# Kernel optimization log

Measured on AMD Instinct MI355X. Metric: run time of the kernel, lower is better.

The kernel has to match this reference:

```python
import jax, jax.numpy as jnp
import numpy as np

K = 16          # num clusters
DZ = 64         # dim_zt == dim_zi (required by decoder matmul)
DT = 1024       # treatment feature dim (dim_t)
NT = 2048       # number of treatments == dim_x (columns of input_ins)
NI = 4096       # number of instances
MU_P_WT = 5.0
COS_EPS = 1e-6


def setup_inputs() -> dict:
    key = jax.random.key(0)
    ks = jax.random.split(key, 12)
    s = 0.02
    return {
        "input_ins": jax.random.uniform(ks[0], (NI, NT), dtype=jnp.float32),
        "input_treat": jax.random.normal(ks[1], (NT, DT), dtype=jnp.float32),
        # nn.Linear params (torch layout: W [out, in], y = x @ W.T + b)
        "W_mu_zt": jax.random.normal(ks[2], (DZ, DT)) * s,
        "b_mu_zt": jnp.zeros((DZ,), jnp.float32),
        "W_lv_zt": jax.random.normal(ks[3], (DZ, DT)) * s,
        "b_lv_zt": jnp.zeros((DZ,), jnp.float32),
        "W_arec": jax.random.normal(ks[4], (DT, DZ)) * s,
        "b_arec": jnp.zeros((DT,), jnp.float32),
        "W_mu_zi": jax.random.normal(ks[5], (DZ, NT)) * s,
        "b_mu_zi": jnp.zeros((DZ,), jnp.float32),
        "W_lv_zi": jax.random.normal(ks[6], (DZ, NT)) * s,
        "b_lv_zi": jnp.zeros((DZ,), jnp.float32),
        "mu_p_zt": jax.random.normal(ks[7], (K, DZ), dtype=jnp.float32),
        "logvar_p_zt": jnp.ones((K, DZ), jnp.float32),
        "W_y1": jax.random.normal(ks[8], (K * DZ, DZ)) * s,
        "b_y1": jnp.zeros((K * DZ,), jnp.float32),
        "W_y2": jax.random.normal(ks[9], (1, K * DZ)) * s,
        "b_y2": jnp.zeros((1,), jnp.float32),
    }


def reference(input_ins, input_treat, W_mu_zt, b_mu_zt, W_lv_zt, b_lv_zt,
              W_arec, b_arec, W_mu_zi, b_mu_zi, W_lv_zi, b_lv_zi,
              mu_p_zt, logvar_p_zt, W_y1, b_y1, W_y2, b_y2):
    # encode_t (eval mode: zt_sample = mu_zt)
    mu_zt = input_treat @ W_mu_zt.T + b_mu_zt           # [NT, DZ]
    logvar_zt = input_treat @ W_lv_zt.T + b_lv_zt       # [NT, DZ]
    zt = mu_zt

    # compute_qc (cosine similarity vs scaled cluster centers, *10)
    centers = MU_P_WT * mu_p_zt                          # [K, DZ]
    num = zt @ centers.T                                 # [NT, K]
    denom = jnp.maximum(
        jnp.linalg.norm(zt, axis=1, keepdims=True) * jnp.linalg.norm(centers, axis=1)[None, :],
        COS_EPS)
    qc_raw = 10.0 * num / denom                          # [NT, K]
    cates = jax.nn.softmax(qc_raw, axis=1)               # forward softmaxes qc once
    c_sample = jax.nn.softmax(cates, axis=1)             # encode_i (eval) softmaxes again

    # encode_i, vectorized over K clusters: (input_ins * cates_k) @ W.T + b
    # fused einsum avoids materializing the [K, NI, NT] masked inputs
    mu_zi = jnp.einsum('nt,tk,dt->knd', input_ins, c_sample, W_mu_zi) + b_mu_zi       # [K, NI, DZ]
    logvar_zi = jnp.einsum('nt,tk,dt->knd', input_ins, c_sample, W_lv_zi) + b_lv_zi   # [K, NI, DZ]
    zi = mu_zi  # eval-mode reparameterize

    # a_reconstby_zt
    a_reconst = jax.nn.sigmoid(zt @ W_arec.T + b_arec)   # [NT, DT]

    # decoder: sum_k sigmoid(zi_k @ zt.T) * cates_k
    logits = jnp.einsum('knd,td->knt', zi, zt)           # [K, NI, NT]
    a_pred = jnp.einsum('knt,tk->nt', jax.nn.sigmoid(logits), c_sample)  # [NI, NT]

    # predictY
    zi_all = jnp.transpose(zi, (1, 0, 2)).reshape(zi.shape[1], K * DZ)   # cat over k, dim=1
    a_zt = input_ins @ zt                                # [NI, DZ]
    rep_w1 = a_zt @ W_y1.T + b_y1                        # [NI, K*DZ]
    pred_y2 = zi_all @ W_y2.T + b_y2                     # [NI, 1]
    # diag(rep_w1 @ zi_all.T) == rowwise dot product (no NIxNI matmul)
    mu_y = jnp.sum(rep_w1 * zi_all, axis=1, keepdims=True) + pred_y2     # [NI, 1]
    logvar_y = jnp.ones_like(mu_y)

    return (mu_zt, logvar_zt, mu_p_zt, logvar_p_zt, cates, mu_zi, logvar_zi,
            zi, a_pred, mu_y, logvar_y, a_reconst)
```

## Files before the change

kernel.cpp:

```cpp
#include <hip/hip_runtime.h>

typedef unsigned short ushort_t;
typedef unsigned int   uint32;
typedef __attribute__((ext_vector_type(8))) short short8;
typedef __attribute__((ext_vector_type(4))) float f32x4;

#define DEV __device__ __forceinline__

#define KC 16
#define DZ 64
#define DT 1024
#define NT 2048
#define NI 4096
#define KD 1024

#define O_MU_ZT   0
#define O_LV_ZT   131072
#define O_MU_P    262144
#define O_LV_P    263168
#define O_CATES   264192
#define O_MU_ZI   296960
#define O_LV_ZI   4491264
#define O_ZI      8685568
#define O_APRED   12879872
#define O_MU_Y    21268480
#define O_LV_Y    21272576
#define O_AREC    21276672

#define WSF_ZT   0
#define WSF_C    131072
#define WSF_CT   163840
#define WSF_AZT  196608
#define WSF_END  458752
#define WSU_ZTB  0
#define WSU_BC   131072
#define WSU_ZIB  4325376
#define WSU_INSB 8519680
#define WSU_ZHT  16908288
#define WSU_ZLT  17039360
#define WSU_END  17170432

DEV ushort_t f2b(float f){
  uint32 u = __float_as_uint(f);
  u += 0x7fffu + ((u >> 16) & 1u);
  return (ushort_t)(u >> 16);
}
DEV uint32 pk(float lo, float hi){
  return (__float_as_uint(hi) & 0xffff0000u) | (__float_as_uint(lo) >> 16);
}
DEV float wred64(float v){
#pragma unroll
  for (int m = 32; m; m >>= 1) v += __shfl_xor(v, m, 64);
  return v;
}
DEV float fastrcp(float x){ return __builtin_amdgcn_rcpf(x); }
DEV void gl2lds16(ushort_t* l, const ushort_t* g){
  __builtin_amdgcn_global_load_lds(
      (const __attribute__((address_space(1))) unsigned int*)g,
      (__attribute__((address_space(3))) unsigned int*)l, 16, 0, 0);
}

__global__ __launch_bounds__(512) void k_encode_t(
    const float* __restrict__ treat, const float* __restrict__ Wmu,
    const float* __restrict__ bmu, const float* __restrict__ Wlv,
    const float* __restrict__ blv, float* __restrict__ out,
    float* __restrict__ ws_zt)
{
  __shared__ float rowsh[8 * DT];
  const int n0 = blockIdx.x * 8, tid = threadIdx.x;
  const float4* src = (const float4*)(treat + (size_t)n0 * DT);
#pragma unroll
  for (int i = 0; i < 4; ++i)
    ((float4*)rowsh)[tid + i * 512] = src[tid + i * 512];
  __syncthreads();
  const int j = tid & 127, half = tid >> 7;
  const bool isMu = j < 64;
  const int jj = j & 63;
  const float* W = (isMu ? Wmu : Wlv) + (size_t)jj * DT;
  const float bias = isMu ? bmu[jj] : blv[jj];
  float a0 = bias, a1 = bias;
  const float4* w4 = (const float4*)W;
  const float4* r0 = (const float4*)&rowsh[(half*2 + 0) * DT];
  const float4* r1 = (const float4*)&rowsh[(half*2 + 1) * DT];
#pragma unroll 4
  for (int i = 0; i < DT / 4; ++i){
    float4 wv = w4[i];
    float4 v0 = r0[i], v1 = r1[i];
    a0 += wv.x*v0.x + wv.y*v0.y + wv.z*v0.z + wv.w*v0.w;
    a1 += wv.x*v1.x + wv.y*v1.y + wv.z*v1.z + wv.w*v1.w;
  }
  float acc[2] = {a0, a1};
#pragma unroll
  for (int r = 0; r < 2; ++r){
    const int row = n0 + half*2 + r;
    if (isMu){ out[O_MU_ZT + row*DZ + jj] = acc[r]; ws_zt[row*DZ + jj] = acc[r]; }
    else     { out[O_LV_ZT + row*DZ + jj] = acc[r]; }
  }
}

__global__ __launch_bounds__(256) void k_qc(
    const float* __restrict__ mu_p, const float* __restrict__ ws_zt,
    float* __restrict__ out, float* __restrict__ ws_c, float* __restrict__ ws_cT)
{
  const int tid = threadIdx.x, lane = tid & 63;
  const int row = blockIdx.x * 4 + (tid >> 6);
  const float z = ws_zt[row * DZ + lane];
  const float nz = sqrtf(wred64(z * z));
  float myqc = 0.f;
#pragma unroll
  for (int k = 0; k < KC; ++k){
    float cv  = 5.f * mu_p[k * DZ + lane];
    float dot = wred64(z * cv);
    float nc2 = wred64(cv * cv);
    float qc  = 10.f * dot / fmaxf(nz * sqrtf(nc2), 1e-6f);
    if (lane == k) myqc = qc;
  }
  float mx = myqc;
#pragma unroll
  for (int m = 8; m; m >>= 1) mx = fmaxf(mx, __shfl_xor(mx, m, 16));
  float e = __expf(myqc - mx);
  float s = e;
#pragma unroll
  for (int m = 8; m; m >>= 1) s += __shfl_xor(s, m, 16);
  float cates = e / s;
  float mx2 = cates;
#pragma unroll
  for (int m = 8; m; m >>= 1) mx2 = fmaxf(mx2, __shfl_xor(mx2, m, 16));
  float e2 = __expf(cates - mx2);
  float s2 = e2;
#pragma unroll
  for (int m = 8; m; m >>= 1) s2 += __shfl_xor(s2, m, 16);
  float c2 = e2 / s2;
  if (lane < KC){
    out[O_CATES + row * KC + lane] = cates;
    ws_c[row * KC + lane] = c2;
    ws_cT[lane * NT + row] = c2;
  }
}

__global__ __launch_bounds__(256) void k_prep(
    const float* __restrict__ Wmu, const float* __restrict__ Wlv,
    const float* __restrict__ cT, const float* __restrict__ zt,
    const float* __restrict__ ins, const float* __restrict__ Wy1,
    ushort_t* __restrict__ Bc, ushort_t* __restrict__ ztb,
    ushort_t* __restrict__ insb,
    ushort_t* __restrict__ zhT, ushort_t* __restrict__ zlT,
    float* __restrict__ w1T,
    const float* __restrict__ mu_p, const float* __restrict__ lv_p,
    float* __restrict__ out)
{
  const int bx = blockIdx.x, tid = threadIdx.x;
  if (bx < 2048){
    const int j = bx;
    const bool isMu = j < KD;
    const int kk = (j & (KD-1)) >> 6, d = j & 63;
    const float* W = (isMu ? Wmu : Wlv) + (size_t)d * NT;
    const float* c = cT + (size_t)kk * NT;
    const int t = tid * 8;
    float4 w0 = *(const float4*)(W + t), w1 = *(const float4*)(W + t + 4);
    float4 c0 = *(const float4*)(c + t), c1 = *(const float4*)(c + t + 4);
    ushort_t v[8];
    v[0]=f2b(w0.x*c0.x); v[1]=f2b(w0.y*c0.y); v[2]=f2b(w0.z*c0.z); v[3]=f2b(w0.w*c0.w);
    v[4]=f2b(w1.x*c1.x); v[5]=f2b(w1.y*c1.y); v[6]=f2b(w1.z*c1.z); v[7]=f2b(w1.w*c1.w);
    *(uint4*)(Bc + (size_t)j * NT + t) = *(uint4*)v;
  } else if (bx < 2080){
    const int g = (bx - 2048) * 256 + tid;
    const int base = g * 16;
    const float4* src = (const float4*)(zt + base);
    float4 z0 = src[0], z1 = src[1], z2 = src[2], z3 = src[3];
    ushort_t v[16];
    v[0]=f2b(z0.x); v[1]=f2b(z0.y); v[2]=f2b(z0.z); v[3]=f2b(z0.w);
    v[4]=f2b(z1.x); v[5]=f2b(z1.y); v[6]=f2b(z1.z); v[7]=f2b(z1.w);
    v[8]=f2b(z2.x); v[9]=f2b(z2.y); v[10]=f2b(z2.z); v[11]=f2b(z2.w);
    v[12]=f2b(z3.x); v[13]=f2b(z3.y); v[14]=f2b(z3.z); v[15]=f2b(z3.w);
    *(uint4*)(ztb + base) = *(uint4*)&v[0];
    *(uint4*)(ztb + base + 8) = *(uint4*)&v[8];
  } else if (bx < 2084){
    const int i = (bx - 2080) * 256 + tid;
    out[O_MU_P + i] = mu_p[i];
    out[O_LV_P + i] = lv_p[i];
  } else if (bx < 4132){
    const int g = (bx - 2084) * 256 + tid;
    const int base = g * 16;
    const float4* src = (const float4*)(ins + base);
    float4 z0 = src[0], z1 = src[1], z2 = src[2], z3 = src[3];
    ushort_t v[16];
    v[0]=f2b(z0.x); v[1]=f2b(z0.y); v[2]=f2b(z0.z); v[3]=f2b(z0.w);
    v[4]=f2b(z1.x); v[5]=f2b(z1.y); v[6]=f2b(z1.z); v[7]=f2b(z1.w);
    v[8]=f2b(z2.x); v[9]=f2b(z2.y); v[10]=f2b(z2.z); v[11]=f2b(z2.w);
    v[12]=f2b(z3.x); v[13]=f2b(z3.y); v[14]=f2b(z3.z); v[15]=f2b(z3.w);
    *(uint4*)(insb + base) = *(uint4*)&v[0];
    *(uint4*)(insb + base + 8) = *(uint4*)&v[8];
  } else if (bx < 4164){
    __shared__ float zsh[64 * 65];
    const int t0 = (bx - 4132) * 64;
#pragma unroll
    for (int jj = 0; jj < 16; ++jj){
      const int idx = jj * 256 + tid;
      const int t = idx >> 6, d = idx & 63;
      zsh[t * 65 + d] = zt[(size_t)(t0 + t) * DZ + d];
    }
    __syncthreads();
    const int d = tid >> 2, tq = tid & 3;
    ushort_t vh[16], vl[16];
#pragma unroll
    for (int i = 0; i < 16; ++i){
      const float f = zsh[(tq * 16 + i) * 65 + d];
      const uint32 u = __float_as_uint(f);
      vh[i] = (ushort_t)(u >> 16);
      const float hf = __uint_as_float(u & 0xffff0000u);
      vl[i] = (ushort_t)(__float_as_uint(f - hf) >> 16);
    }
    *(uint4*)(zhT + (size_t)d * NT + t0 + tq * 16)     = *(uint4*)&vh[0];
    *(uint4*)(zhT + (size_t)d * NT + t0 + tq * 16 + 8) = *(uint4*)&vh[8];
    *(uint4*)(zlT + (size_t)d * NT + t0 + tq * 16)     = *(uint4*)&vl[0];
    *(uint4*)(zlT + (size_t)d * NT + t0 + tq * 16 + 8) = *(uint4*)&vl[8];
  } else {
    __shared__ float wsh[64 * 65];
    const int j0 = (bx - 4164) * 64;
#pragma unroll
    for (int jj = 0; jj < 16; ++jj){
      const int idx = jj * 256 + tid;
      const int r = idx >> 6, d = idx & 63;
      wsh[r * 65 + d] = Wy1[(size_t)(j0 + r) * DZ + d];
    }
    __syncthreads();
    const int d = tid >> 2, q = tid & 3;
    float v[16];
#pragma unroll
    for (int i = 0; i < 16; ++i) v[i] = wsh[(q*16 + i)*65 + d];
#pragma unroll
    for (int i = 0; i < 4; ++i){
      float4 o; o.x = v[i*4]; o.y = v[i*4+1]; o.z = v[i*4+2]; o.w = v[i*4+3];
      *(float4*)&w1T[(size_t)d * KD + j0 + q*16 + i*4] = o;
    }
  }
}

__global__ __launch_bounds__(256) void k_encode_i(
    const ushort_t* __restrict__ insb, const ushort_t* __restrict__ Bc,
    const float* __restrict__ bmu, const float* __restrict__ blv,
    float* __restrict__ out, ushort_t* __restrict__ zib)
{
  __shared__ ushort_t As[128*64];
  __shared__ ushort_t Bs[128*64];
  const int tid = threadIdx.x;
  const int j0 = blockIdx.x * 128, n0 = blockIdx.y * 128;
  const int w = tid >> 6, lane = tid & 63;
  const int wm = w & 1, wn = w >> 1;
  const int l16 = lane & 15, quad = lane >> 4;

  const int srow = tid >> 3, schunk = (tid & 7) ^ (srow & 7);
  const ushort_t* aSrc = insb + (size_t)(n0 + srow) * NT + schunk * 8;
  const ushort_t* bSrc = Bc  + (size_t)(j0 + srow) * NT + schunk * 8;
  ushort_t* aDst = &As[tid * 8];
  ushort_t* bDst = &Bs[tid * 8];

  f32x4 acc[4][4] = {};

  for (int kt = 0; kt < NT/64; ++kt){
    const ushort_t* ak = aSrc + kt * 64;
    const ushort_t* bk = bSrc + kt * 64;
#pragma unroll
    for (int i = 0; i < 4; ++i){
      gl2lds16(aDst + i * 2048, ak + (size_t)i * 32 * NT);
      gl2lds16(bDst + i * 2048, bk + (size_t)i * 32 * NT);
    }
    __syncthreads();
#pragma unroll
    for (int ks = 0; ks < 2; ++ks){
      const int rsw = ((ks*4 + quad) ^ (l16 & 7)) * 8;
      short8 af[4], bf[4];
#pragma unroll
      for (int mf = 0; mf < 4; ++mf)
        af[mf] = *(const short8*)&As[(wm*64 + mf*16 + l16)*64 + rsw];
#pragma unroll
      for (int nf = 0; nf < 4; ++nf)
        bf[nf] = *(const short8*)&Bs[(wn*64 + nf*16 + l16)*64 + rsw];
#pragma unroll
      for (int mf = 0; mf < 4; ++mf)
#pragma unroll
        for (int nf = 0; nf < 4; ++nf)
          acc[mf][nf] = __builtin_amdgcn_mfma_f32_16x16x32_bf16(af[mf], bf[nf], acc[mf][nf], 0, 0, 0);
    }
    __syncthreads();
  }

  const int colW = j0 + wn * 64;
  const bool isMu = colW < KD;
  const int kk = (colW & (KD - 1)) >> 6;
  const float* bias = isMu ? bmu : blv;
  const size_t zbase = (size_t)kk * (NI * DZ);
#pragma unroll
  for (int mf = 0; mf < 4; ++mf){
    const int r = n0 + wm*64 + mf*16 + quad*4;
#pragma unroll
    for (int nf = 0; nf < 4; ++nf){
      const int d = nf*16 + l16;
      const float bv = bias[d];
#pragma unroll
      for (int reg = 0; reg < 4; ++reg){
        float v = acc[mf][nf][reg] + bv;
        size_t idx = zbase + (size_t)(r + reg)*DZ + d;
        if (isMu){
          out[O_MU_ZI + idx] = v;
          out[O_ZI + idx] = v;
          zib[idx] = f2b(v);
        } else {
          out[O_LV_ZI + idx] = v;
        }
      }
    }
  }
}

__global__ __launch_bounds__(256) void k_decoder(
    const ushort_t* __restrict__ ztb, const ushort_t* __restrict__ zib,
    const float* __restrict__ ws_c, float* __restrict__ out)
{
  __shared__ ushort_t Zt[64*64];
  __shared__ ushort_t Zi[128*64];
  __shared__ float ct[64*17];
  const int tid = threadIdx.x;
  const int t0 = blockIdx.x * 64, n0 = blockIdx.y * 128;
  const int w = tid >> 6, lane = tid & 63;
  const int wm = w & 1, wn = w >> 1;
  const int l16 = lane & 15, quad = lane >> 4;
  const int zr = tid >> 2, zq = tid & 3;
  const int ir = tid >> 1, ih = tid & 1;
  {
    const uint4* src = (const uint4*)(ztb + (size_t)(t0 + zr)*DZ + zq*16);
    uint4 z0 = src[0], z1 = src[1];
    ushort_t* dst = &Zt[zr*64];
    *(uint4*)&dst[((zq*2 + 0) ^ (zr & 7)) * 8] = z0;
    *(uint4*)&dst[((zq*2 + 1) ^ (zr & 7)) * 8] = z1;
  }
  for (int i = tid; i < 64*16; i += 256){
    int t = i >> 4, k = i & 15;
    ct[t*17 + k] = ws_c[(size_t)(t0 + t)*KC + k];
  }
  __syncthreads();
  short8 bfh[2][2];
#pragma unroll
  for (int ks = 0; ks < 2; ++ks){
    const int rsw = ((ks*4 + quad) ^ (l16 & 7)) * 8;
#pragma unroll
    for (int nf = 0; nf < 2; ++nf)
      bfh[ks][nf] = *(const short8*)&Zt[(wn*32 + nf*16 + l16)*64 + rsw];
  }
  const ushort_t* iG = zib + (size_t)(n0 + ir)*DZ + ih*32;
  ushort_t* isw = &Zi[ir*64];
  const int sw0 = ((ih*4 + 0) ^ (ir & 7)) * 8;
  const int sw1 = ((ih*4 + 1) ^ (ir & 7)) * 8;
  const int sw2 = ((ih*4 + 2) ^ (ir & 7)) * 8;
  const int sw3 = ((ih*4 + 3) ^ (ir & 7)) * 8;
  uint4 Zr0, Zr1, Zr2, Zr3;
  {
    const uint4* zp = (const uint4*)iG;
    Zr0 = zp[0]; Zr1 = zp[1]; Zr2 = zp[2]; Zr3 = zp[3];
  }
  f32x4 accum[4][2] = {};
  for (int k = 0; k < KC; ++k){
    __syncthreads();
    *(uint4*)&isw[sw0] = Zr0; *(uint4*)&isw[sw1] = Zr1;
    *(uint4*)&isw[sw2] = Zr2; *(uint4*)&isw[sw3] = Zr3;
    __syncthreads();
    if (k < KC - 1){
      const uint4* zp = (const uint4*)(iG + (size_t)(k+1)*(NI*DZ));
      Zr0 = zp[0]; Zr1 = zp[1]; Zr2 = zp[2]; Zr3 = zp[3];
    }
    f32x4 s[4][2] = {};
#pragma unroll
    for (int ks = 0; ks < 2; ++ks){
      const int rsw = ((ks*4 + quad) ^ (l16 & 7)) * 8;
      short8 af[4];
#pragma unroll
      for (int mf = 0; mf < 4; ++mf)
        af[mf] = *(const short8*)&Zi[(wm*64 + mf*16 + l16)*64 + rsw];
#pragma unroll
      for (int mf = 0; mf < 4; ++mf)
#pragma unroll
        for (int nf = 0; nf < 2; ++nf)
          s[mf][nf] = __builtin_amdgcn_mfma_f32_16x16x32_bf16(af[mf], bfh[ks][nf], s[mf][nf], 0, 0, 0);
    }
#pragma unroll
    for (int nf = 0; nf < 2; ++nf){
      const float cv = ct[(wn*32 + nf*16 + l16)*17 + k];
#pragma unroll
      for (int mf = 0; mf < 4; ++mf)
#pragma unroll
        for (int reg = 0; reg < 4; ++reg)
          accum[mf][nf][reg] += cv * fastrcp(1.f + __expf(-s[mf][nf][reg]));
    }
  }
#pragma unroll
  for (int mf = 0; mf < 4; ++mf){
    const int r = n0 + wm*64 + mf*16 + quad*4;
#pragma unroll
    for (int nf = 0; nf < 2; ++nf){
      const int col = t0 + wn*32 + nf*16 + l16;
#pragma unroll
      for (int reg = 0; reg < 4; ++reg)
        out[O_APRED + (size_t)(r + reg)*NT + col] = accum[mf][nf][reg];
    }
  }
}

__global__ __launch_bounds__(512) void k_arec(
    const float* __restrict__ ws_zt, const float* __restrict__ W,
    const float* __restrict__ bias, float* __restrict__ out)
{
  __shared__ float zsh[8 * DZ];
  const int n0 = blockIdx.x * 8, tid = threadIdx.x;
  if (tid < 128)
    ((float4*)zsh)[tid] = ((const float4*)(ws_zt + (size_t)n0 * DZ))[tid];
  __syncthreads();
#pragma unroll
  for (int jo = 0; jo < 2; ++jo){
    const int j = jo*512 + tid;
    const float4* w4 = (const float4*)(W + (size_t)j * DZ);
    const float b = bias[j];
    float acc[8];
#pragma unroll
    for (int r = 0; r < 8; ++r) acc[r] = b;
#pragma unroll
    for (int i = 0; i < 16; ++i){
      float4 wv = w4[i];
#pragma unroll
      for (int r = 0; r < 8; ++r){
        const float* z = &zsh[r*DZ + i*4];
        acc[r] += wv.x*z[0] + wv.y*z[1] + wv.z*z[2] + wv.w*z[3];
      }
    }
#pragma unroll
    for (int r = 0; r < 8; ++r)
      out[O_AREC + (size_t)(n0 + r)*DT + j] = fastrcp(1.f + __expf(-acc[r]));
  }
}

__global__ __launch_bounds__(512) void k_azt(
    const float* __restrict__ ins, const ushort_t* __restrict__ zhT,
    const ushort_t* __restrict__ zlT, float* __restrict__ azt)
{
  __shared__ float red[16*64];
  const int tid = threadIdx.x;
  const int n0 = blockIdx.x * 16;
  const int w = tid >> 6, lane = tid & 63;
  const int kh = w >> 2, wd = w & 3;
  const int l16 = lane & 15, quad = lane >> 4;
  const float* aRow = ins + (size_t)(n0 + l16) * NT + kh * 1024 + quad * 8;
  const ushort_t* bh = zhT + (size_t)(wd * 16 + l16) * NT + kh * 1024 + quad * 8;
  const ushort_t* bl = zlT + (size_t)(wd * 16 + l16) * NT + kh * 1024 + quad * 8;
  f32x4 acc = {};
#pragma unroll 4
  for (int kt = 0; kt < 16; ++kt){
#pragma unroll
    for (int ks = 0; ks < 2; ++ks){
      const int ko = kt * 64 + ks * 32;
      float4 a0 = *(const float4*)(aRow + ko);
      float4 a1 = *(const float4*)(aRow + ko + 4);
      uint32 u0 = __float_as_uint(a0.x), u1 = __float_as_uint(a0.y);
      uint32 u2 = __float_as_uint(a0.z), u3 = __float_as_uint(a0.w);
      uint32 u4 = __float_as_uint(a1.x), u5 = __float_as_uint(a1.y);
      uint32 u6 = __float_as_uint(a1.z), u7 = __float_as_uint(a1.w);
      uint4 H, L;
      H.x = (u1 & 0xffff0000u) | (u0 >> 16);
      H.y = (u3 & 0xffff0000u) | (u2 >> 16);
      H.z = (u5 & 0xffff0000u) | (u4 >> 16);
      H.w = (u7 & 0xffff0000u) | (u6 >> 16);
      float l0 = a0.x - __uint_as_float(u0 & 0xffff0000u);
      float l1 = a0.y - __uint_as_float(u1 & 0xffff0000u);
      float l2 = a0.z - __uint_as_float(u2 & 0xffff0000u);
      float l3 = a0.w - __uint_as_float(u3 & 0xffff0000u);
      float l4 = a1.x - __uint_as_float(u4 & 0xffff0000u);
      float l5 = a1.y - __uint_as_float(u5 & 0xffff0000u);
      float l6 = a1.z - __uint_as_float(u6 & 0xffff0000u);
      float l7 = a1.w - __uint_as_float(u7 & 0xffff0000u);
      L.x = pk(l0, l1); L.y = pk(l2, l3); L.z = pk(l4, l5); L.w = pk(l6, l7);
      short8 ah = *(short8*)&H, al = *(short8*)&L;
      short8 bh8 = *(const short8*)(bh + ko);
      short8 bl8 = *(const short8*)(bl + ko);
      acc = __builtin_amdgcn_mfma_f32_16x16x32_bf16(ah, bh8, acc, 0, 0, 0);
      acc = __builtin_amdgcn_mfma_f32_16x16x32_bf16(al, bh8, acc, 0, 0, 0);
      acc = __builtin_amdgcn_mfma_f32_16x16x32_bf16(ah, bl8, acc, 0, 0, 0);
    }
  }
  const int col = wd * 16 + l16;
  if (kh == 1){
#pragma unroll
    for (int reg = 0; reg < 4; ++reg)
      red[(quad*4 + reg)*64 + col] = acc[reg];
  }
  __syncthreads();
  if (kh == 0){
#pragma unroll
    for (int reg = 0; reg < 4; ++reg)
      azt[(size_t)(n0 + quad*4 + reg) * DZ + col] = acc[reg] + red[(quad*4 + reg)*64 + col];
  }
}

__global__ __launch_bounds__(512) void k_muy(
    const float* __restrict__ azt, const float* __restrict__ w1T,
    const float* __restrict__ by1, const float* __restrict__ Wy2,
    const float* __restrict__ by2, const float* __restrict__ zi_out,
    float* __restrict__ out)
{
  __shared__ float sazt[16][DZ];
  __shared__ float sred[8][16];
  const int tid = threadIdx.x;
  const int n0 = blockIdx.x * 16;
  for (int i = tid; i < 16*DZ; i += 512)
    sazt[i >> 6][i & 63] = azt[(size_t)(n0 + (i >> 6))*DZ + (i & 63)];
  __syncthreads();
  const int w = tid >> 6, lane = tid & 63;
  const int jA = w*128 + lane, jB = jA + 64;
  float repA[16] = {}, repB[16] = {};
#pragma unroll 4
  for (int d4 = 0; d4 < 16; ++d4){
    const float* wrow = w1T + (size_t)(d4*4) * KD;
    const float wa0 = wrow[jA],        wb0 = wrow[jB];
    const float wa1 = wrow[KD + jA],   wb1 = wrow[KD + jB];
    const float wa2 = wrow[2*KD + jA], wb2 = wrow[2*KD + jB];
    const float wa3 = wrow[3*KD + jA], wb3 = wrow[3*KD + jB];
#pragma unroll
    for (int n = 0; n < 16; ++n){
      float4 av = *(const float4*)&sazt[n][d4*4];
      repA[n] += av.x*wa0 + av.y*wa1 + av.z*wa2 + av.w*wa3;
      repB[n] += av.x*wb0 + av.y*wb1 + av.z*wb2 + av.w*wb3;
    }
  }
  const float addA = by1[jA] + Wy2[jA];
  const float addB = by1[jB] + Wy2[jB];
  const size_t zbA = (size_t)(w*2    ) * (NI*DZ) + lane;
  const size_t zbB = (size_t)(w*2 + 1) * (NI*DZ) + lane;
#pragma unroll
  for (int n = 0; n < 16; ++n){
    const size_t ro = (size_t)(n0 + n) * DZ;
    float p = (repA[n] + addA) * zi_out[zbA + ro]
            + (repB[n] + addB) * zi_out[zbB + ro];
    p = wred64(p);
    if (lane == 0) sred[w][n] = p;
  }
  __syncthreads();
  if (tid < 16){
    float s = by2[0];
#pragma unroll
    for (int ww = 0; ww < 8; ++ww) s += sred[ww][tid];
    out[O_MU_Y + n0 + tid] = s;
    out[O_LV_Y + n0 + tid] = 1.0f;
  }
}

extern "C" void kernel_launch(void* const* d_in, const int* in_sizes, int n_in,
                              void* d_out, int out_size, void* d_ws, size_t ws_size,
                              hipStream_t stream)
{
  (void)in_sizes; (void)n_in; (void)out_size; (void)ws_size;
  const float* ins   = (const float*)d_in[0];
  const float* treat = (const float*)d_in[1];
  const float* Wmzt  = (const float*)d_in[2];
  const float* bmzt  = (const float*)d_in[3];
  const float* Wlzt  = (const float*)d_in[4];
  const float* blzt  = (const float*)d_in[5];
  const float* Warec = (const float*)d_in[6];
  const float* barec = (const float*)d_in[7];
  const float* Wmzi  = (const float*)d_in[8];
  const float* bmzi  = (const float*)d_in[9];
  const float* Wlzi  = (const float*)d_in[10];
  const float* blzi  = (const float*)d_in[11];
  const float* mu_p  = (const float*)d_in[12];
  const float* lv_p  = (const float*)d_in[13];
  const float* Wy1   = (const float*)d_in[14];
  const float* by1   = (const float*)d_in[15];
  const float* Wy2   = (const float*)d_in[16];
  const float* by2   = (const float*)d_in[17];
  float* out = (float*)d_out;
  float* wsf = (float*)d_ws;
  ushort_t* wsu = (ushort_t*)(wsf + WSF_END);

  float* ws_zt  = wsf + WSF_ZT;
  float* ws_c   = wsf + WSF_C;
  float* ws_cT  = wsf + WSF_CT;
  float* ws_azt = wsf + WSF_AZT;
  ushort_t* ztb  = wsu + WSU_ZTB;
  ushort_t* Bc   = wsu + WSU_BC;
  ushort_t* zib  = wsu + WSU_ZIB;
  ushort_t* insb = wsu + WSU_INSB;
  ushort_t* zhT  = wsu + WSU_ZHT;
  ushort_t* zlT  = wsu + WSU_ZLT;
  float* w1T     = (float*)(wsu + WSU_END);

  k_encode_t<<<NT/8, 512, 0, stream>>>(treat, Wmzt, bmzt, Wlzt, blzt, out, ws_zt);
  k_qc      <<<NT/4, 256, 0, stream>>>(mu_p, ws_zt, out, ws_c, ws_cT);
  k_prep    <<<4180, 256, 0, stream>>>(Wmzi, Wlzi, ws_cT, ws_zt, ins, Wy1, Bc, ztb, insb, zhT, zlT, w1T, mu_p, lv_p, out);
  k_encode_i<<<dim3(16, 32), 256, 0, stream>>>(insb, Bc, bmzi, blzi, out, zib);
  k_decoder <<<dim3(32, 32), 256, 0, stream>>>(ztb, zib, ws_c, out);
  k_arec    <<<NT/8, 512, 0, stream>>>(ws_zt, Warec, barec, out);
  k_azt     <<<NI/16, 512, 0, stream>>>(ins, zhT, zlT, ws_azt);
  k_muy     <<<NI/16, 512, 0, stream>>>(ws_azt, w1T, by1, Wy2, by2, out + O_ZI, out);
}
```

Baseline: 413.9 us.

## Compute encode_t with split-bf16 MFMA and move input-only prep ahead

The FP32 scalar GEMV-style encode_t kernel is replaced by a bf16x3 (hi/lo split) MFMA kernel that processes 16 rows per block, with a K-split across two wave groups reduced through LDS. Weights are pre-split into hi/lo bf16 buffers by a new k_prep0 kernel. That kernel also takes over the conversion of input_ins and the other input-only prep from the old monolithic prep kernel, which is split in two so the input-independent work runs before encode_t. This aims to cut encode_t's FP32 ALU cost, at the price of an extra launch and some precision loss from the three-term split.

After: 376.4 us. 9.1% less time.

```diff
diff --git a/kernel.cpp b/kernel.cpp
--- a/kernel.cpp
+++ b/kernel.cpp
@@ -38,7 +38,9 @@
 #define WSU_INSB 8519680
 #define WSU_ZHT  16908288
 #define WSU_ZLT  17039360
-#define WSU_END  17170432
+#define WSU_WBH  17170432
+#define WSU_WBL  17301504
+#define WSU_END  17432576
 
 DEV ushort_t f2b(float f){
   uint32 u = __float_as_uint(f);
@@ -60,41 +62,141 @@
       (__attribute__((address_space(3))) unsigned int*)l, 16, 0, 0);
 }
 
+__global__ __launch_bounds__(256) void k_prep0(
+    const float* __restrict__ ins, const float* __restrict__ Wy1,
+    const float* __restrict__ Wmzt, const float* __restrict__ Wlzt,
+    const float* __restrict__ mu_p, const float* __restrict__ lv_p,
+    ushort_t* __restrict__ insb, float* __restrict__ w1T,
+    ushort_t* __restrict__ wbh, ushort_t* __restrict__ wbl,
+    float* __restrict__ out)
+{
+  const int bx = blockIdx.x, tid = threadIdx.x;
+  if (bx < 2048){
+    const int g = bx * 256 + tid;
+    const int base = g * 16;
+    const float4* src = (const float4*)(ins + base);
+    float4 z0 = src[0], z1 = src[1], z2 = src[2], z3 = src[3];
+    ushort_t v[16];
+    v[0]=f2b(z0.x); v[1]=f2b(z0.y); v[2]=f2b(z0.z); v[3]=f2b(z0.w);
+    v[4]=f2b(z1.x); v[5]=f2b(z1.y); v[6]=f2b(z1.z); v[7]=f2b(z1.w);
+    v[8]=f2b(z2.x); v[9]=f2b(z2.y); v[10]=f2b(z2.z); v[11]=f2b(z2.w);
+    v[12]=f2b(z3.x); v[13]=f2b(z3.y); v[14]=f2b(z3.z); v[15]=f2b(z3.w);
+    *(uint4*)(insb + base) = *(uint4*)&v[0];
+    *(uint4*)(insb + base + 8) = *(uint4*)&v[8];
+  } else if (bx < 2064){
+    __shared__ float wsh[64 * 65];
+    const int j0 = (bx - 2048) * 64;
+#pragma unroll
+    for (int jj = 0; jj < 16; ++jj){
+      const int idx = jj * 256 + tid;
+      const int r = idx >> 6, d = idx & 63;
+      wsh[r * 65 + d] = Wy1[(size_t)(j0 + r) * DZ + d];
+    }
+    __syncthreads();
+    const int d = tid >> 2, q = tid & 3;
+    float v[16];
+#pragma unroll
+    for (int i = 0; i < 16; ++i) v[i] = wsh[(q*16 + i)*65 + d];
+#pragma unroll
+    for (int i = 0; i < 4; ++i){
+      float4 o; o.x = v[i*4]; o.y = v[i*4+1]; o.z = v[i*4+2]; o.w = v[i*4+3];
+      *(float4*)&w1T[(size_t)d * KD + j0 + q*16 + i*4] = o;
+    }
+  } else if (bx < 2128){
+    const int idx = (bx - 2064) * 2048 + tid * 8;
+    const int row = idx >> 10, k = idx & 1023;
+    const float* src = (row < 64 ? Wmzt + (size_t)row * DT
+                                 : Wlzt + (size_t)(row - 64) * DT) + k;
+    float4 a0 = *(const float4*)src, a1 = *(const float4*)(src + 4);
+    float f[8] = {a0.x, a0.y, a0.z, a0.w, a1.x, a1.y, a1.z, a1.w};
+    ushort_t vh[8], vl[8];
+#pragma unroll
+    for (int i = 0; i < 8; ++i){
+      const uint32 u = __float_as_uint(f[i]);
+      vh[i] = (ushort_t)(u >> 16);
+      const float hf = __uint_as_float(u & 0xffff0000u);
+      vl[i] = (ushort_t)(__float_as_uint(f[i] - hf) >> 16);
+    }
+    *(uint4*)(wbh + (size_t)row * DT + k) = *(uint4*)vh;
+    *(uint4*)(wbl + (size_t)row * DT + k) = *(uint4*)vl;
+  } else {
+    const int i = (bx - 2128) * 256 + tid;
+    out[O_MU_P + i] = mu_p[i];
+    out[O_LV_P + i] = lv_p[i];
+  }
+}
+
 __global__ __launch_bounds__(512) void k_encode_t(
-    const float* __restrict__ treat, const float* __restrict__ Wmu,
-    const float* __restrict__ bmu, const float* __restrict__ Wlv,
+    const float* __restrict__ treat, const ushort_t* __restrict__ wbh,
+    const ushort_t* __restrict__ wbl, const float* __restrict__ bmu,
     const float* __restrict__ blv, float* __restrict__ out,
     float* __restrict__ ws_zt)
 {
-  __shared__ float rowsh[8 * DT];
-  const int n0 = blockIdx.x * 8, tid = threadIdx.x;
-  const float4* src = (const float4*)(treat + (size_t)n0 * DT);
-#pragma unroll
-  for (int i = 0; i < 4; ++i)
-    ((float4*)rowsh)[tid + i * 512] = src[tid + i * 512];
+  __shared__ float red[16 * 128];
+  const int tid = threadIdx.x;
+  const int n0 = blockIdx.x * 16;
+  const int w = tid >> 6, lane = tid & 63;
+  const int kh = w >> 2, wd = w & 3;
+  const int l16 = lane & 15, quad = lane >> 4;
+  const float* aRow = treat + (size_t)(n0 + l16) * DT + kh * 512 + quad * 8;
+  const int colA = wd * 16 + l16;
+  const ushort_t* bhA = wbh + (size_t)colA * DT + kh * 512 + quad * 8;
+  const ushort_t* blA = wbl + (size_t)colA * DT + kh * 512 + quad * 8;
+  const ushort_t* bhB = wbh + (size_t)(colA + 64) * DT + kh * 512 + quad * 8;
+  const ushort_t* blB = wbl + (size_t)(colA + 64) * DT + kh * 512 + quad * 8;
+  f32x4 accA = {}, accB = {};
+#pragma unroll 4
+  for (int kt = 0; kt < 16; ++kt){
+    const int ko = kt * 32;
+    float4 a0 = *(const float4*)(aRow + ko);
+    float4 a1 = *(const float4*)(aRow + ko + 4);
+    uint32 u0 = __float_as_uint(a0.x), u1 = __float_as_uint(a0.y);
+    uint32 u2 = __float_as_uint(a0.z), u3 = __float_as_uint(a0.w);
+    uint32 u4 = __float_as_uint(a1.x), u5 = __float_as_uint(a1.y);
+    uint32 u6 = __float_as_uint(a1.z), u7 = __float_as_uint(a1.w);
+    uint4 H, L;
+    H.x = (u1 & 0xffff0000u) | (u0 >> 16);
+    H.y = (u3 & 0xffff0000u) | (u2 >> 16);
+    H.z = (u5 & 0xffff0000u) | (u4 >> 16);
+    H.w = (u7 & 0xffff0000u) | (u6 >> 16);
+    float l0 = a0.x - __uint_as_float(u0 & 0xffff0000u);
+    float l1 = a0.y - __uint_as_float(u1 & 0xffff0000u);
+    float l2 = a0.z - __uint_as_float(u2 & 0xffff0000u);
+    float l3 = a0.w - __uint_as_float(u3 & 0xffff0000u);
+    float l4 = a1.x - __uint_as_float(u4 & 0xffff0000u);
+    float l5 = a1.y - __uint_as_float(u5 & 0xffff0000u);
+    float l6 = a1.z - __uint_as_float(u6 & 0xffff0000u);
+    float l7 = a1.w - __uint_as_float(u7 & 0xffff0000u);
+    L.x = pk(l0, l1); L.y = pk(l2, l3); L.z = pk(l4, l5); L.w = pk(l6, l7);
+    short8 ah = *(short8*)&H, al = *(short8*)&L;
+    short8 hA = *(const short8*)(bhA + ko), lA = *(const short8*)(blA + ko);
+    short8 hB = *(const short8*)(bhB + ko), lB = *(const short8*)(blB + ko);
+    accA = __builtin_amdgcn_mfma_f32_16x16x32_bf16(ah, hA, accA, 0, 0, 0);
+    accA = __builtin_amdgcn_mfma_f32_16x16x32_bf16(al, hA, accA, 0, 0, 0);
+    accA = __builtin_amdgcn_mfma_f32_16x16x32_bf16(ah, lA, accA, 0, 0, 0);
+    accB = __builtin_amdgcn_mfma_f32_16x16x32_bf16(ah, hB, accB, 0, 0, 0);
+    accB = __builtin_amdgcn_mfma_f32_16x16x32_bf16(al, hB, accB, 0, 0, 0);
+    accB = __builtin_amdgcn_mfma_f32_16x16x32_bf16(ah, lB, accB, 0, 0, 0);
+  }
+  if (kh == 1){
+#pragma unroll
+    for (int reg = 0; reg < 4; ++reg){
+      red[(quad*4 + reg)*128 + colA]      = accA[reg];
+      red[(quad*4 + reg)*128 + colA + 64] = accB[reg];
+    }
+  }
   __syncthreads();
-  const int j = tid & 127, half = tid >> 7;
-  const bool isMu = j < 64;
-  const int jj = j & 63;
-  const float* W = (isMu ? Wmu : Wlv) + (size_t)jj * DT;
-  const float bias = isMu ? bmu[jj] : blv[jj];
-  float a0 = bias, a1 = bias;
-  const float4* w4 = (const float4*)W;
-  const float4* r0 = (const float4*)&rowsh[(half*2 + 0) * DT];
-  const float4* r1 = (const float4*)&rowsh[(half*2 + 1) * DT];
-#pragma unroll 4
-  for (int i = 0; i < DT / 4; ++i){
-    float4 wv = w4[i];
-    float4 v0 = r0[i], v1 = r1[i];
-    a0 += wv.x*v0.x + wv.y*v0.y + wv.z*v0.z + wv.w*v0.w;
-    a1 += wv.x*v1.x + wv.y*v1.y + wv.z*v1.z + wv.w*v1.w;
-  }
-  float acc[2] = {a0, a1};
-#pragma unroll
-  for (int r = 0; r < 2; ++r){
-    const int row = n0 + half*2 + r;
-    if (isMu){ out[O_MU_ZT + row*DZ + jj] = acc[r]; ws_zt[row*DZ + jj] = acc[r]; }
-    else     { out[O_LV_ZT + row*DZ + jj] = acc[r]; }
+  if (kh == 0){
+    const float bA = bmu[colA], bB = blv[colA];
+#pragma unroll
+    for (int reg = 0; reg < 4; ++reg){
+      const int row = n0 + quad*4 + reg;
+      const float vA = accA[reg] + red[(quad*4 + reg)*128 + colA] + bA;
+      const float vB = accB[reg] + red[(quad*4 + reg)*128 + colA + 64] + bB;
+      out[O_MU_ZT + row*DZ + colA] = vA;
+      ws_zt[row*DZ + colA] = vA;
+      out[O_LV_ZT + row*DZ + colA] = vB;
+    }
   }
 }
 
@@ -138,16 +240,11 @@
   }
 }
 
-__global__ __launch_bounds__(256) void k_prep(
+__global__ __launch_bounds__(256) void k_prep1(
     const float* __restrict__ Wmu, const float* __restrict__ Wlv,
     const float* __restrict__ cT, const float* __restrict__ zt,
-    const float* __restrict__ ins, const float* __restrict__ Wy1,
     ushort_t* __restrict__ Bc, ushort_t* __restrict__ ztb,
-    ushort_t* __restrict__ insb,
-    ushort_t* __restrict__ zhT, ushort_t* __restrict__ zlT,
-    float* __restrict__ w1T,
-    const float* __restrict__ mu_p, const float* __restrict__ lv_p,
-    float* __restrict__ out)
+    ushort_t* __restrict__ zhT, ushort_t* __restrict__ zlT)
 {
   const int bx = blockIdx.x, tid = threadIdx.x;
   if (bx < 2048){
@@ -175,25 +272,9 @@
     v[12]=f2b(z3.x); v[13]=f2b(z3.y); v[14]=f2b(z3.z); v[15]=f2b(z3.w);
     *(uint4*)(ztb + base) = *(uint4*)&v[0];
     *(uint4*)(ztb + base + 8) = *(uint4*)&v[8];
-  } else if (bx < 2084){
-    const int i = (bx - 2080) * 256 + tid;
-    out[O_MU_P + i] = mu_p[i];
-    out[O_LV_P + i] = lv_p[i];
-  } else if (bx < 4132){
-    const int g = (bx - 2084) * 256 + tid;
-    const int base = g * 16;
-    const float4* src = (const float4*)(ins + base);
-    float4 z0 = src[0], z1 = src[1], z2 = src[2], z3 = src[3];
-    ushort_t v[16];
-    v[0]=f2b(z0.x); v[1]=f2b(z0.y); v[2]=f2b(z0.z); v[3]=f2b(z0.w);
-    v[4]=f2b(z1.x); v[5]=f2b(z1.y); v[6]=f2b(z1.z); v[7]=f2b(z1.w);
-    v[8]=f2b(z2.x); v[9]=f2b(z2.y); v[10]=f2b(z2.z); v[11]=f2b(z2.w);
-    v[12]=f2b(z3.x); v[13]=f2b(z3.y); v[14]=f2b(z3.z); v[15]=f2b(z3.w);
-    *(uint4*)(insb + base) = *(uint4*)&v[0];
-    *(uint4*)(insb + base + 8) = *(uint4*)&v[8];
-  } else if (bx < 4164){
+  } else {
     __shared__ float zsh[64 * 65];
-    const int t0 = (bx - 4132) * 64;
+    const int t0 = (bx - 2080) * 64;
 #pragma unroll
     for (int jj = 0; jj < 16; ++jj){
       const int idx = jj * 256 + tid;
@@ -215,25 +296,6 @@
     *(uint4*)(zhT + (size_t)d * NT + t0 + tq * 16 + 8) = *(uint4*)&vh[8];
     *(uint4*)(zlT + (size_t)d * NT + t0 + tq * 16)     = *(uint4*)&vl[0];
     *(uint4*)(zlT + (size_t)d * NT + t0 + tq * 16 + 8) = *(uint4*)&vl[8];
-  } else {
-    __shared__ float wsh[64 * 65];
-    const int j0 = (bx - 4164) * 64;
-#pragma unroll
-    for (int jj = 0; jj < 16; ++jj){
-      const int idx = jj * 256 + tid;
-      const int r = idx >> 6, d = idx & 63;
-      wsh[r * 65 + d] = Wy1[(size_t)(j0 + r) * DZ + d];
-    }
-    __syncthreads();
-    const int d = tid >> 2, q = tid & 3;
-    float v[16];
-#pragma unroll
-    for (int i = 0; i < 16; ++i) v[i] = wsh[(q*16 + i)*65 + d];
-#pragma unroll
-    for (int i = 0; i < 4; ++i){
-      float4 o; o.x = v[i*4]; o.y = v[i*4+1]; o.z = v[i*4+2]; o.w = v[i*4+3];
-      *(float4*)&w1T[(size_t)d * KD + j0 + q*16 + i*4] = o;
-    }
   }
 }
 
@@ -588,11 +650,14 @@
   ushort_t* insb = wsu + WSU_INSB;
   ushort_t* zhT  = wsu + WSU_ZHT;
   ushort_t* zlT  = wsu + WSU_ZLT;
+  ushort_t* wbh  = wsu + WSU_WBH;
+  ushort_t* wbl  = wsu + WSU_WBL;
   float* w1T     = (float*)(wsu + WSU_END);
 
-  k_encode_t<<<NT/8, 512, 0, stream>>>(treat, Wmzt, bmzt, Wlzt, blzt, out, ws_zt);
+  k_prep0   <<<2132, 256, 0, stream>>>(ins, Wy1, Wmzt, Wlzt, mu_p, lv_p, insb, w1T, wbh, wbl, out);
+  k_encode_t<<<NT/16, 512, 0, stream>>>(treat, wbh, wbl, bmzt, blzt, out, ws_zt);
   k_qc      <<<NT/4, 256, 0, stream>>>(mu_p, ws_zt, out, ws_c, ws_cT);
-  k_prep    <<<4180, 256, 0, stream>>>(Wmzi, Wlzi, ws_cT, ws_zt, ins, Wy1, Bc, ztb, insb, zhT, zlT, w1T, mu_p, lv_p, out);
+  k_prep1   <<<2112, 256, 0, stream>>>(Wmzi, Wlzi, ws_cT, ws_zt, Bc, ztb, zhT, zlT);
   k_encode_i<<<dim3(16, 32), 256, 0, stream>>>(insb, Bc, bmzi, blzi, out, zib);
   k_decoder <<<dim3(32, 32), 256, 0, stream>>>(ztb, zib, ws_c, out);
   k_arec    <<<NT/8, 512, 0, stream>>>(ws_zt, Warec, barec, out);
```
